# Optimization experiments

Hardware: AMD Instinct MI355X
Metric: run time of the kernel (lower is better)

Reference implementation:

```python
import jax, jax.numpy as jnp
import numpy as np

SQRT_N = 32
SQRT_D = 32
B, N, D = 32, SQRT_N ** 2, SQRT_D ** 2  # batch, seq, d_model
LN_EPS = 1e-5


def _perm(x, s):
    # rearrange '... (m n) -> ... (n m)' with n = s
    shp = x.shape
    return x.reshape(*shp[:-1], -1, s).swapaxes(-1, -2).reshape(shp)


def _blockdiag_matmul(x, w):
    # w: [blocks, n, m]; x viewed as [..., blocks, m]
    s = w.shape[0]
    xv = x.reshape(*x.shape[:-1], s, w.shape[-1])
    return jnp.einsum('bnm,...bm->...bn', w, xv).reshape(x.shape)


def _monarch(x, L, R, s):
    x = _perm(x, s)
    x = _blockdiag_matmul(x, L)
    x = _perm(x, s)
    x = _blockdiag_matmul(x, R)
    return _perm(x, s)


def setup_inputs() -> dict:
    key = jax.random.key(0)
    ks = jax.random.split(key, 12)
    p = lambda k, s: (jax.random.normal(ks[k], (s, s, s), dtype=jnp.float32) * (1.0 / np.sqrt(s)))
    return {
        'x': jax.random.normal(ks[0], (B, N, D), dtype=jnp.float32),
        'm1_L': p(1, SQRT_N), 'm1_R': p(2, SQRT_N),
        'm2_L': p(3, SQRT_N), 'm2_R': p(4, SQRT_N),
        'm3_L': p(5, SQRT_D), 'm3_R': p(6, SQRT_D),
        'm4_L': p(7, SQRT_D), 'm4_R': p(8, SQRT_D),
        'n_kernel': jax.random.normal(ks[9], (SQRT_D ** 2, SQRT_N ** 2), dtype=jnp.float32),
        'd_kernel': jax.random.normal(ks[10], (1, SQRT_D ** 2), dtype=jnp.float32),
        'ln_gamma': jnp.ones((SQRT_D ** 2,), dtype=jnp.float32),
        'ln_beta': jnp.zeros((SQRT_D ** 2,), dtype=jnp.float32),
    }


def reference(x, m1_L, m1_R, m2_L, m2_R, m3_L, m3_R, m4_L, m4_R,
              n_kernel, d_kernel, ln_gamma, ln_beta):
    b, n, d = x.shape
    n2, d2 = SQRT_N ** 2, SQRT_D ** 2
    # pad sequence dim to sqrt_n^2
    x = jnp.pad(x, ((0, 0), (0, n2 - n), (0, 0)))
    # sequence (n) mixing, operating on [b, d, n2]
    xt = x.swapaxes(-1, -2)
    xt = _monarch(xt, m1_L, m1_R, SQRT_N)
    xt = jax.nn.relu(n_kernel * xt)
    xt = _monarch(xt, m2_L, m2_R, SQRT_N)
    x_tilde = xt.swapaxes(-1, -2)[:, :n, :]
    # pad feature dim to sqrt_d^2
    x_tilde = jnp.pad(x_tilde, ((0, 0), (0, 0), (0, d2 - x_tilde.shape[-1])))
    # feature (d) mixing
    y = _monarch(x_tilde, m3_L, m3_R, SQRT_D)
    y = jax.nn.relu(d_kernel * y)
    y = _monarch(y, m4_L, m4_R, SQRT_D)
    y = y[..., :d]
    # residual + LayerNorm over last dim (biased variance, eps=1e-5)
    h = y + x_tilde
    mu = jnp.mean(h, axis=-1, keepdims=True)
    var = jnp.mean(jnp.square(h - mu), axis=-1, keepdims=True)
    return (h - mu) * jax.lax.rsqrt(var + LN_EPS) * ln_gamma + ln_beta
```

## Files before the change

kernel.cpp:

```cpp
#include <hip/hip_runtime.h>


#define TILE_ELEMS (1024 * 32)

struct EpiNone {
  __device__ __forceinline__ void operator()(float2&, int) const {}
};
struct EpiReluDK {
  const float* dk;
  __device__ __forceinline__ void operator()(float2& v, int n) const {
    float w = dk[n];
    float a = v.x * w, b = v.y * w;
    v.x = a > 0.f ? a : 0.f;
    v.y = b > 0.f ? b : 0.f;
  }
};

template <class Epi>
__device__ __forceinline__ void monarch32(float* tile,
                                          const float* __restrict__ L,
                                          const float* __restrict__ R,
                                          int tid, const Epi epi) {
  const int l2 = (tid & 15) << 1;
  const int pr = (tid >> 4) & 31;
  const int h  = tid >> 9;
  const int pb = pr << 5;
  const int blA = l2 ^ (((pr >> 2) & 7) << 2);
  const int blB = l2 ^ ((pr & 7) << 2);
  {
    float2 X[32];
#pragma unroll
    for (int j = 0; j < 32; ++j)
      X[j] = *(const float2*)&tile[(j << 10) + pb + (blA ^ ((j & 7) << 2))];
    __syncthreads();
    const float* Lp = L + (pr << 10) + (h << 9);
#pragma unroll
    for (int i = 0; i < 16; ++i) {
      const float4* w4 = (const float4*)(Lp + (i << 5));
      float ax = 0.f, ay = 0.f;
#pragma unroll
      for (int q = 0; q < 8; ++q) {
        float4 w = w4[q];
        ax = fmaf(w.x, X[4 * q + 0].x, ax); ay = fmaf(w.x, X[4 * q + 0].y, ay);
        ax = fmaf(w.y, X[4 * q + 1].x, ax); ay = fmaf(w.y, X[4 * q + 1].y, ay);
        ax = fmaf(w.z, X[4 * q + 2].x, ax); ay = fmaf(w.z, X[4 * q + 2].y, ay);
        ax = fmaf(w.w, X[4 * q + 3].x, ax); ay = fmaf(w.w, X[4 * q + 3].y, ay);
      }
      const int c = (h << 4) + i;
      float2 o; o.x = ax; o.y = ay;
      *(float2*)&tile[(c << 10) + pb + (blA ^ ((c & 7) << 2))] = o;
    }
  }
  __syncthreads();
  {
    float2 M[32];
#pragma unroll
    for (int m = 0; m < 32; ++m)
      M[m] = *(const float2*)&tile[(pr << 10) + (m << 5) + (blB ^ ((m >> 2) << 2))];
    __syncthreads();
    const float* Rp = R + (pr << 10) + (h << 9);
#pragma unroll
    for (int i = 0; i < 16; ++i) {
      const float4* w4 = (const float4*)(Rp + (i << 5));
      float ax = 0.f, ay = 0.f;
#pragma unroll
      for (int q = 0; q < 8; ++q) {
        float4 w = w4[q];
        ax = fmaf(w.x, M[4 * q + 0].x, ax); ay = fmaf(w.x, M[4 * q + 0].y, ay);
        ax = fmaf(w.y, M[4 * q + 1].x, ax); ay = fmaf(w.y, M[4 * q + 1].y, ay);
        ax = fmaf(w.z, M[4 * q + 2].x, ax); ay = fmaf(w.z, M[4 * q + 2].y, ay);
        ax = fmaf(w.w, M[4 * q + 3].x, ax); ay = fmaf(w.w, M[4 * q + 3].y, ay);
      }
      const int u = (h << 4) + i;
      const int n = (u << 5) + pr;
      float2 o; o.x = ax; o.y = ay;
      epi(o, n);
      *(float2*)&tile[(u << 10) + pb + (blA ^ ((u & 7) << 2))] = o;
    }
  }
  __syncthreads();
}

__global__ __launch_bounds__(1024, 4) void p1_kernel(
    const float* __restrict__ x, const float* __restrict__ m1L,
    const float* __restrict__ m1R, const float* __restrict__ m2L,
    const float* __restrict__ m2R, const float* __restrict__ nk,
    float* __restrict__ xt_out) {
  __shared__ float tile[TILE_ELEMS];
  const int b = blockIdx.y, d0 = blockIdx.x << 5;
  const int tid = (int)threadIdx.x;
  {
    const int g4 = tid & 7, nn = tid >> 3, l4 = g4 << 2;
    const float* xb = x + ((size_t)b << 20) + d0 + l4;
#pragma unroll
    for (int j = 0; j < 8; ++j) {
      const int n = (j << 7) + nn;
      float4 v = *(const float4*)&xb[(size_t)n << 10];
      const int t = ((n >> 2) ^ (n >> 5)) & 7;
      *(float4*)&tile[(n << 5) + (l4 ^ (t << 2))] = v;
    }
  }
  __syncthreads();
  monarch32(tile, m1L, m1R, tid, EpiNone());
  {
    const int q = tid & 31, l = tid >> 5;
    const int bl = l ^ (((q >> 2) & 7) << 2);
    const float* nkr = nk + ((size_t)(d0 + l) << 10);
#pragma unroll
    for (int j = 0; j < 32; ++j) {
      const int n = (j << 5) + q;
      const int a = (j << 10) + (q << 5) + (bl ^ ((j & 7) << 2));
      float v = tile[a] * nkr[n];
      tile[a] = v > 0.f ? v : 0.f;
    }
  }
  __syncthreads();
  monarch32(tile, m2L, m2R, tid, EpiNone());
  {
    const int g4 = tid & 7, nn = tid >> 3, l4 = g4 << 2;
    float* ob = xt_out + ((size_t)b << 20) + d0 + l4;
#pragma unroll
    for (int j = 0; j < 8; ++j) {
      const int n = (j << 7) + nn;
      const int t = ((n >> 2) ^ (n >> 5)) & 7;
      float4 v = *(const float4*)&tile[(n << 5) + (l4 ^ (t << 2))];
      *(float4*)&ob[(size_t)n << 10] = v;
    }
  }
}

__global__ __launch_bounds__(1024, 4) void p2_kernel(
    const float* xt, const float* __restrict__ m3L,
    const float* __restrict__ m3R, const float* __restrict__ m4L,
    const float* __restrict__ m4R, const float* __restrict__ dk,
    const float* __restrict__ gamma, const float* __restrict__ beta,
    float* out) {
  __shared__ float tile[TILE_ELEMS];
  const int b = blockIdx.y, n0 = blockIdx.x << 5;
  const int tid = (int)threadIdx.x;
  const float* xrows = xt + ((((size_t)b << 10) + n0) << 10);
  {
    const int c = tid & 255, lg = tid >> 8;
    const int t = (c ^ (c >> 3)) & 7;
#pragma unroll
    for (int k = 0; k < 8; ++k) {
      const int l = (lg << 3) + k;
      float4 v = *(const float4*)&xrows[((size_t)l << 10) + (c << 2)];
      const int lx = l ^ (t << 2);
      tile[(c << 7) + lx] = v.x;
      tile[(c << 7) + 32 + lx] = v.y;
      tile[(c << 7) + 64 + lx] = v.z;
      tile[(c << 7) + 96 + lx] = v.w;
    }
  }
  __syncthreads();
  EpiReluDK e3; e3.dk = dk;
  monarch32(tile, m3L, m3R, tid, e3);
  monarch32(tile, m4L, m4R, tid, EpiNone());
  {
    const int q = tid & 31, l = tid >> 5;
    const int bl = l ^ (((q >> 2) & 7) << 2);
    const float* xr = xrows + ((size_t)l << 10);
    float hbuf[32];
    float s = 0.f;
#pragma unroll
    for (int j = 0; j < 32; ++j) {
      const int n = (j << 5) + q;
      float hv = tile[(j << 10) + (q << 5) + (bl ^ ((j & 7) << 2))] + xr[n];
      hbuf[j] = hv;
      s += hv;
    }
#pragma unroll
    for (int m = 1; m <= 16; m <<= 1) s += __shfl_xor(s, m);
    const float mu = s * (1.f / 1024.f);
    float vs = 0.f;
#pragma unroll
    for (int j = 0; j < 32; ++j) {
      float d = hbuf[j] - mu;
      vs = fmaf(d, d, vs);
    }
#pragma unroll
    for (int m = 1; m <= 16; m <<= 1) vs += __shfl_xor(vs, m);
    const float rs = rsqrtf(vs * (1.f / 1024.f) + 1e-5f);
    float* orow = out + ((((size_t)b << 10) + n0 + l) << 10);
#pragma unroll
    for (int j = 0; j < 32; ++j) {
      const int n = (j << 5) + q;
      orow[n] = (hbuf[j] - mu) * rs * gamma[n] + beta[n];
    }
  }
}

extern "C" void kernel_launch(void* const* d_in, const int* in_sizes, int n_in,
                              void* d_out, int out_size, void* d_ws, size_t ws_size,
                              hipStream_t stream) {
  (void)in_sizes; (void)n_in; (void)out_size; (void)d_ws; (void)ws_size;
  const float* x   = (const float*)d_in[0];
  const float* m1L = (const float*)d_in[1];
  const float* m1R = (const float*)d_in[2];
  const float* m2L = (const float*)d_in[3];
  const float* m2R = (const float*)d_in[4];
  const float* m3L = (const float*)d_in[5];
  const float* m3R = (const float*)d_in[6];
  const float* m4L = (const float*)d_in[7];
  const float* m4R = (const float*)d_in[8];
  const float* nk  = (const float*)d_in[9];
  const float* dk  = (const float*)d_in[10];
  const float* gam = (const float*)d_in[11];
  const float* bet = (const float*)d_in[12];
  float* out = (float*)d_out;

  dim3 grid(32, 32), block(1024);
  hipLaunchKernelGGL(p1_kernel, grid, block, 0, stream,
                     x, m1L, m1R, m2L, m2R, nk, out);
  hipLaunchKernelGGL(p2_kernel, grid, block, 0, stream,
                     out, m3L, m3R, m4L, m4R, dk, gam, bet, out);
}
```

Baseline: 922.6 us.

## Restructure monarch thread mapping to one column per thread and halve p2 tiles

Rewrites the monarch block-diagonal multiply so each thread handles a single column and all 32 outputs of a block, instead of two columns and half the outputs. It replaces the float2 accumulators with scalar dot products. The feature-mixing kernel now uses 16-row tiles with 512 threads and a new XOR swizzle, doubling its grid. The aim is more weight reuse per thread, lower LDS use per block and better occupancy in p2, at the cost of half as many columns sharing each weight load and a partial unroll of the output loops.

New measurement: 1.324 ms. +43.5%, slower.

```diff
diff --git a/kernel.cpp b/kernel.cpp
--- a/kernel.cpp
+++ b/kernel.cpp
@@ -1,81 +1,73 @@
 #include <hip/hip_runtime.h>
 
 
-#define TILE_ELEMS (1024 * 32)
+__device__ __forceinline__ int cell1(int n, int l) {
+  return (n << 5) + (l ^ ((((n >> 2) ^ (n >> 5)) & 7) << 2));
+}
+__device__ __forceinline__ int cell2(int n, int l) {
+  return (n << 4) + (l ^ (((n >> 1) ^ (n >> 5)) & 15));
+}
+
+__device__ __forceinline__ float dot32(const float* __restrict__ Wrow,
+                                       const float (&X)[32]) {
+  const float4* w4 = reinterpret_cast<const float4*>(Wrow);
+  float acc = 0.f;
+#pragma unroll
+  for (int q = 0; q < 8; ++q) {
+    float4 w = w4[q];
+    acc = fmaf(w.x, X[4 * q + 0], acc);
+    acc = fmaf(w.y, X[4 * q + 1], acc);
+    acc = fmaf(w.z, X[4 * q + 2], acc);
+    acc = fmaf(w.w, X[4 * q + 3], acc);
+  }
+  return acc;
+}
 
 struct EpiNone {
-  __device__ __forceinline__ void operator()(float2&, int) const {}
+  __device__ __forceinline__ void operator()(float&, int) const {}
 };
 struct EpiReluDK {
   const float* dk;
-  __device__ __forceinline__ void operator()(float2& v, int n) const {
-    float w = dk[n];
-    float a = v.x * w, b = v.y * w;
-    v.x = a > 0.f ? a : 0.f;
-    v.y = b > 0.f ? b : 0.f;
+  __device__ __forceinline__ void operator()(float& v, int n) const {
+    float a = v * dk[n];
+    v = a > 0.f ? a : 0.f;
   }
 };
 
-template <class Epi>
-__device__ __forceinline__ void monarch32(float* tile,
-                                          const float* __restrict__ L,
-                                          const float* __restrict__ R,
-                                          int tid, const Epi epi) {
-  const int l2 = (tid & 15) << 1;
-  const int pr = (tid >> 4) & 31;
-  const int h  = tid >> 9;
-  const int pb = pr << 5;
-  const int blA = l2 ^ (((pr >> 2) & 7) << 2);
-  const int blB = l2 ^ ((pr & 7) << 2);
-  {
-    float2 X[32];
-#pragma unroll
-    for (int j = 0; j < 32; ++j)
-      X[j] = *(const float2*)&tile[(j << 10) + pb + (blA ^ ((j & 7) << 2))];
+template <int W16, class Epi>
+__device__ __forceinline__ void monarch(float* tile, const float* __restrict__ L,
+                                        const float* __restrict__ R, int l, int p,
+                                        const Epi epi) {
+  {
+    float X[32];
+#pragma unroll
+    for (int k = 0; k < 32; ++k) {
+      const int n = (k << 5) + p;
+      X[k] = tile[W16 ? cell2(n, l) : cell1(n, l)];
+    }
+    const float* Lp = L + (p << 10);
+#pragma unroll 2
+    for (int c = 0; c < 32; ++c) {
+      const int n = (c << 5) + p;
+      tile[W16 ? cell2(n, l) : cell1(n, l)] = dot32(Lp + (c << 5), X);
+    }
+  }
+  __syncthreads();
+  {
+    float M[32];
+#pragma unroll
+    for (int m = 0; m < 32; ++m) {
+      const int n = (p << 5) + m;
+      M[m] = tile[W16 ? cell2(n, l) : cell1(n, l)];
+    }
     __syncthreads();
-    const float* Lp = L + (pr << 10) + (h << 9);
-#pragma unroll
-    for (int i = 0; i < 16; ++i) {
-      const float4* w4 = (const float4*)(Lp + (i << 5));
-      float ax = 0.f, ay = 0.f;
-#pragma unroll
-      for (int q = 0; q < 8; ++q) {
-        float4 w = w4[q];
-        ax = fmaf(w.x, X[4 * q + 0].x, ax); ay = fmaf(w.x, X[4 * q + 0].y, ay);
-        ax = fmaf(w.y, X[4 * q + 1].x, ax); ay = fmaf(w.y, X[4 * q + 1].y, ay);
-        ax = fmaf(w.z, X[4 * q + 2].x, ax); ay = fmaf(w.z, X[4 * q + 2].y, ay);
-        ax = fmaf(w.w, X[4 * q + 3].x, ax); ay = fmaf(w.w, X[4 * q + 3].y, ay);
-      }
-      const int c = (h << 4) + i;
-      float2 o; o.x = ax; o.y = ay;
-      *(float2*)&tile[(c << 10) + pb + (blA ^ ((c & 7) << 2))] = o;
-    }
-  }
-  __syncthreads();
-  {
-    float2 M[32];
-#pragma unroll
-    for (int m = 0; m < 32; ++m)
-      M[m] = *(const float2*)&tile[(pr << 10) + (m << 5) + (blB ^ ((m >> 2) << 2))];
-    __syncthreads();
-    const float* Rp = R + (pr << 10) + (h << 9);
-#pragma unroll
-    for (int i = 0; i < 16; ++i) {
-      const float4* w4 = (const float4*)(Rp + (i << 5));
-      float ax = 0.f, ay = 0.f;
-#pragma unroll
-      for (int q = 0; q < 8; ++q) {
-        float4 w = w4[q];
-        ax = fmaf(w.x, M[4 * q + 0].x, ax); ay = fmaf(w.x, M[4 * q + 0].y, ay);
-        ax = fmaf(w.y, M[4 * q + 1].x, ax); ay = fmaf(w.y, M[4 * q + 1].y, ay);
-        ax = fmaf(w.z, M[4 * q + 2].x, ax); ay = fmaf(w.z, M[4 * q + 2].y, ay);
-        ax = fmaf(w.w, M[4 * q + 3].x, ax); ay = fmaf(w.w, M[4 * q + 3].y, ay);
-      }
-      const int u = (h << 4) + i;
-      const int n = (u << 5) + pr;
-      float2 o; o.x = ax; o.y = ay;
-      epi(o, n);
-      *(float2*)&tile[(u << 10) + pb + (blA ^ ((u & 7) << 2))] = o;
+    const float* Rp = R + (p << 10);
+#pragma unroll 2
+    for (int u = 0; u < 32; ++u) {
+      float acc = dot32(Rp + (u << 5), M);
+      const int n = (u << 5) + p;
+      epi(acc, n);
+      tile[W16 ? cell2(n, l) : cell1(n, l)] = acc;
     }
   }
   __syncthreads();
@@ -86,7 +78,7 @@
     const float* __restrict__ m1R, const float* __restrict__ m2L,
     const float* __restrict__ m2R, const float* __restrict__ nk,
     float* __restrict__ xt_out) {
-  __shared__ float tile[TILE_ELEMS];
+  __shared__ float tile[1024 * 32];
   const int b = blockIdx.y, d0 = blockIdx.x << 5;
   const int tid = (int)threadIdx.x;
   {
@@ -96,78 +88,74 @@
     for (int j = 0; j < 8; ++j) {
       const int n = (j << 7) + nn;
       float4 v = *(const float4*)&xb[(size_t)n << 10];
-      const int t = ((n >> 2) ^ (n >> 5)) & 7;
-      *(float4*)&tile[(n << 5) + (l4 ^ (t << 2))] = v;
-    }
-  }
-  __syncthreads();
-  monarch32(tile, m1L, m1R, tid, EpiNone());
-  {
-    const int q = tid & 31, l = tid >> 5;
-    const int bl = l ^ (((q >> 2) & 7) << 2);
-    const float* nkr = nk + ((size_t)(d0 + l) << 10);
-#pragma unroll
+      *(float4*)&tile[cell1(n, l4)] = v;
+    }
+  }
+  __syncthreads();
+  const int l = tid & 31, p = tid >> 5;
+  monarch<0>(tile, m1L, m1R, l, p, EpiNone());
+  {
+    const int q = tid & 31, ld = tid >> 5;
+    const float* nkr = nk + ((size_t)(d0 + ld) << 10);
+#pragma unroll 4
     for (int j = 0; j < 32; ++j) {
       const int n = (j << 5) + q;
-      const int a = (j << 10) + (q << 5) + (bl ^ ((j & 7) << 2));
+      const int a = cell1(n, ld);
       float v = tile[a] * nkr[n];
       tile[a] = v > 0.f ? v : 0.f;
     }
   }
   __syncthreads();
-  monarch32(tile, m2L, m2R, tid, EpiNone());
+  monarch<0>(tile, m2L, m2R, l, p, EpiNone());
   {
     const int g4 = tid & 7, nn = tid >> 3, l4 = g4 << 2;
     float* ob = xt_out + ((size_t)b << 20) + d0 + l4;
 #pragma unroll
     for (int j = 0; j < 8; ++j) {
       const int n = (j << 7) + nn;
-      const int t = ((n >> 2) ^ (n >> 5)) & 7;
-      float4 v = *(const float4*)&tile[(n << 5) + (l4 ^ (t << 2))];
+      float4 v = *(const float4*)&tile[cell1(n, l4)];
       *(float4*)&ob[(size_t)n << 10] = v;
     }
   }
 }
 
-__global__ __launch_bounds__(1024, 4) void p2_kernel(
+__global__ __launch_bounds__(512, 4) void p2_kernel(
     const float* xt, const float* __restrict__ m3L,
     const float* __restrict__ m3R, const float* __restrict__ m4L,
     const float* __restrict__ m4R, const float* __restrict__ dk,
     const float* __restrict__ gamma, const float* __restrict__ beta,
     float* out) {
-  __shared__ float tile[TILE_ELEMS];
-  const int b = blockIdx.y, n0 = blockIdx.x << 5;
+  __shared__ float tile[1024 * 16];
+  const int b = blockIdx.y, n0 = blockIdx.x << 4;
   const int tid = (int)threadIdx.x;
   const float* xrows = xt + ((((size_t)b << 10) + n0) << 10);
   {
-    const int c = tid & 255, lg = tid >> 8;
-    const int t = (c ^ (c >> 3)) & 7;
-#pragma unroll
-    for (int k = 0; k < 8; ++k) {
-      const int l = (lg << 3) + k;
-      float4 v = *(const float4*)&xrows[((size_t)l << 10) + (c << 2)];
-      const int lx = l ^ (t << 2);
-      tile[(c << 7) + lx] = v.x;
-      tile[(c << 7) + 32 + lx] = v.y;
-      tile[(c << 7) + 64 + lx] = v.z;
-      tile[(c << 7) + 96 + lx] = v.w;
-    }
-  }
-  __syncthreads();
-  EpiReluDK e3; e3.dk = dk;
-  monarch32(tile, m3L, m3R, tid, e3);
-  monarch32(tile, m4L, m4R, tid, EpiNone());
-  {
-    const int q = tid & 31, l = tid >> 5;
-    const int bl = l ^ (((q >> 2) & 7) << 2);
-    const float* xr = xrows + ((size_t)l << 10);
-    float hbuf[32];
+    const int c5 = tid & 31, lr = tid >> 5;
+    const float* xr = xrows + ((size_t)lr << 10);
+#pragma unroll
+    for (int j = 0; j < 8; ++j) {
+      const int d = (j << 7) + (c5 << 2);
+      float4 v = *(const float4*)&xr[d];
+      tile[cell2(d + 0, lr)] = v.x;
+      tile[cell2(d + 1, lr)] = v.y;
+      tile[cell2(d + 2, lr)] = v.z;
+      tile[cell2(d + 3, lr)] = v.w;
+    }
+  }
+  __syncthreads();
+  const int l = tid & 15, p = tid >> 4;
+  monarch<1>(tile, m3L, m3R, l, p, EpiReluDK{dk});
+  monarch<1>(tile, m4L, m4R, l, p, EpiNone());
+  {
+    const int q = tid & 31, lr = tid >> 5;
+    const float* xr = xrows + ((size_t)lr << 10);
+    float hb[32];
     float s = 0.f;
 #pragma unroll
     for (int j = 0; j < 32; ++j) {
       const int n = (j << 5) + q;
-      float hv = tile[(j << 10) + (q << 5) + (bl ^ ((j & 7) << 2))] + xr[n];
-      hbuf[j] = hv;
+      float hv = tile[cell2(n, lr)] + xr[n];
+      hb[j] = hv;
       s += hv;
     }
 #pragma unroll
@@ -176,17 +164,17 @@
     float vs = 0.f;
 #pragma unroll
     for (int j = 0; j < 32; ++j) {
-      float d = hbuf[j] - mu;
+      float d = hb[j] - mu;
       vs = fmaf(d, d, vs);
     }
 #pragma unroll
     for (int m = 1; m <= 16; m <<= 1) vs += __shfl_xor(vs, m);
     const float rs = rsqrtf(vs * (1.f / 1024.f) + 1e-5f);
-    float* orow = out + ((((size_t)b << 10) + n0 + l) << 10);
-#pragma unroll
+    float* orow = out + ((((size_t)b << 10) + n0 + lr) << 10);
+#pragma unroll 4
     for (int j = 0; j < 32; ++j) {
       const int n = (j << 5) + q;
-      orow[n] = (hbuf[j] - mu) * rs * gamma[n] + beta[n];
+      orow[n] = (hb[j] - mu) * rs * gamma[n] + beta[n];
     }
   }
 }
@@ -210,9 +198,8 @@
   const float* bet = (const float*)d_in[12];
   float* out = (float*)d_out;
 
-  dim3 grid(32, 32), block(1024);
-  hipLaunchKernelGGL(p1_kernel, grid, block, 0, stream,
+  hipLaunchKernelGGL(p1_kernel, dim3(32, 32), dim3(1024), 0, stream,
                      x, m1L, m1R, m2L, m2R, nk, out);
-  hipLaunchKernelGGL(p2_kernel, grid, block, 0, stream,
+  hipLaunchKernelGGL(p2_kernel, dim3(64, 32), dim3(512), 0, stream,
                      out, m3L, m3R, m4L, m4R, dk, gam, bet, out);
 }
```
